# Optimization experiments

Hardware: AMD Instinct MI355X
Metric: run time of the kernel (lower is better)

The kernel has to match this reference:

```python
import jax, jax.numpy as jnp
import numpy as np

N_NODES = 100000
N_GRAPHS = 512


def gcn_conv(x, W, b, src, dst, n):
    # PyG GCNConv: h = x @ W; add self-loops; sym-normalize; scatter-add to dst; + bias
    h = x @ W
    loop = jnp.arange(n, dtype=src.dtype)
    s = jnp.concatenate([src, loop])
    d = jnp.concatenate([dst, loop])
    deg = jax.ops.segment_sum(jnp.ones_like(d, dtype=h.dtype), d, num_segments=n)
    dinv = jnp.where(deg > 0, jax.lax.rsqrt(deg), 0.0)
    norm = dinv[s] * dinv[d]               # [E+N]
    msg = h[s] * norm[:, None]             # gather + scale
    out = jax.ops.segment_sum(msg, d, num_segments=n)
    return out + b


def setup_inputs() -> dict:
    key = jax.random.key(0)
    ks = jax.random.split(key, 12)
    F_in, H, C = 128, 128, 10
    x = jax.random.normal(ks[0], (N_NODES, F_in), dtype=jnp.float32)
    edge_index = jax.random.randint(ks[1], (2, 3200000), 0, N_NODES, dtype=jnp.int64)
    batch = jnp.sort(jax.random.randint(ks[2], (N_NODES,), 0, N_GRAPHS, dtype=jnp.int64))
    def glorot(k, fi, fo):
        s = jnp.sqrt(6.0 / (fi + fo))
        return jax.random.uniform(k, (fi, fo), dtype=jnp.float32, minval=-s, maxval=s)
    return {
        "x": x, "edge_index": edge_index, "batch": batch,
        "W_in": glorot(ks[3], F_in, H), "b_in": jnp.zeros((H,), jnp.float32),
        "W_h0": glorot(ks[4], H, H), "b_h0": jnp.zeros((H,), jnp.float32),
        "W_h1": glorot(ks[5], H, H), "b_h1": jnp.zeros((H,), jnp.float32),
        "W_out": glorot(ks[6], H, C), "b_out": jnp.zeros((C,), jnp.float32),
    }


def reference(x, edge_index, batch, W_in, b_in, W_h0, b_h0, W_h1, b_h1, W_out, b_out):
    src, dst = edge_index[0], edge_index[1]
    n = x.shape[0]
    h = jax.nn.relu(gcn_conv(x, W_in, b_in, src, dst, n))
    h = jax.nn.relu(gcn_conv(h, W_h0, b_h0, src, dst, n))
    h = jax.nn.relu(gcn_conv(h, W_h1, b_h1, src, dst, n))
    h = gcn_conv(h, W_out, b_out, src, dst, n)
    # global_mean_pool over graph ids
    sums = jax.ops.segment_sum(h, batch, num_segments=N_GRAPHS)
    cnts = jax.ops.segment_sum(jnp.ones((n,), h.dtype), batch, num_segments=N_GRAPHS)
    pooled = sums / jnp.maximum(cnts, 1.0)[:, None]
    return jax.nn.log_softmax(pooled, axis=-1)
```

## Files before the change

### kernel.cpp

```cpp
#include <hip/hip_runtime.h>
#include <math.h>

#define TPB 256
#define MAXDEG 80
#define SHIFT 8
#define BNODES 256
#define EPB 4096
#define QB 32
#define LSTR 136

typedef short bf16x8 __attribute__((ext_vector_type(8)));
typedef float f32x4 __attribute__((ext_vector_type(4)));

__device__ inline unsigned short f2bf(float f) {
    unsigned u = __float_as_uint(f);
    return (unsigned short)((u + 0x7fffu + ((u >> 16) & 1u)) >> 16);
}
__device__ inline float bflo(unsigned u) { return __uint_as_float(u << 16); }
__device__ inline float bfhi(unsigned u) { return __uint_as_float(u & 0xffff0000u); }


__global__ __launch_bounds__(TPB) void p1_k(const int* __restrict__ src,
                                            const int* __restrict__ dst,
                                            int* __restrict__ cntmat,
                                            int* __restrict__ buckets,
                                            int E, int nb, int nblk1) {
    __shared__ int lcur[512];
    int tid = threadIdx.x, blk = blockIdx.x;
    for (int b = tid; b < nb; b += TPB) lcur[b] = 0;
    __syncthreads();
    int e0 = blk * EPB;
    int m = E - e0; if (m > EPB) m = EPB;
    for (int i = tid; i < m; i += TPB) {
        int d = dst[e0 + i];
        int s = src[e0 + i];
        int b = d >> SHIFT;
        int pos = atomicAdd(&lcur[b], 1);
        if (pos < QB)
            buckets[((size_t)b * nblk1 + blk) * QB + pos] = (s << SHIFT) | (d & (BNODES - 1));
    }
    __syncthreads();
    for (int b = tid; b < nb; b += TPB) {
        int c = lcur[b];
        cntmat[blk * nb + b] = c < QB ? c : QB;
    }
}


__global__ __launch_bounds__(TPB) void p2_k(const int* __restrict__ cntmat,
                                            const int* __restrict__ buckets,
                                            int* __restrict__ csr,
                                            int* __restrict__ deg,
                                            float* __restrict__ dinv, int n, int nb, int nblk1,
                                            const float* __restrict__ W0,
                                            const float* __restrict__ W1,
                                            const float* __restrict__ W2,
                                            const float* __restrict__ W3,
                                            unsigned short* __restrict__ T0,
                                            unsigned short* __restrict__ T1,
                                            unsigned short* __restrict__ T2,
                                            unsigned short* __restrict__ T3,
                                            float* __restrict__ pool,
                                            int* __restrict__ cnt, int ng) {
    int b = blockIdx.x, tid = threadIdx.x;
    if (b >= nb) {
        int widx = b - nb;
        if (widx < 3) {
            const float* W = widx == 0 ? W0 : (widx == 1 ? W1 : W2);
            unsigned short* T = widx == 0 ? T0 : (widx == 1 ? T1 : T2);
            for (int idx = tid; idx < 16384; idx += TPB) {
                int nn = idx >> 7, kk = idx & 127;
                T[idx] = f2bf(W[kk * 128 + nn]);
            }
        } else {
            for (int idx = tid; idx < 2048; idx += TPB) {
                int nn = idx >> 7, kk = idx & 127;
                T3[idx] = nn < 10 ? f2bf(W3[kk * 10 + nn]) : (unsigned short)0;
            }
            for (int i = tid; i < ng * 10; i += TPB) pool[i] = 0.f;
            for (int i = tid; i < ng; i += TPB) cnt[i] = 0;
        }
        return;
    }
    __shared__ int lcnt[BNODES];
    __shared__ int cnts[784];
    lcnt[tid] = 0;
    for (int blk = tid; blk < nblk1; blk += TPB) cnts[blk] = cntmat[blk * nb + b];
    __syncthreads();
    const int* bp = buckets + (size_t)b * nblk1 * QB;
    int vb = b << SHIFT;
    int tot = nblk1 * QB;
    for (int j = tid; j < tot; j += TPB) {
        int blk = j / QB;
        int i = j - blk * QB;
        if (i < cnts[blk]) {
            int rec = bp[(size_t)blk * QB + i];
            int dl = rec & (BNODES - 1);
            int pos = atomicAdd(&lcnt[dl], 1);
            if (pos < MAXDEG) csr[(size_t)(vb + dl) * MAXDEG + pos] = rec >> SHIFT;
        }
    }
    __syncthreads();
    int v = vb + tid;
    if (v < n) {
        int c = lcnt[tid];
        deg[v] = c < MAXDEG ? c : MAXDEG;
        dinv[v] = rsqrtf((float)(c + 1));
    }
}


__device__ __forceinline__ void mfma_tile(const unsigned short* Hs,
                                          const unsigned short* __restrict__ WT,
                                          const float* __restrict__ dinv,
                                          unsigned short* __restrict__ gout,
                                          int vb, int n, int w, int l) {
    f32x4 acc[2][8];
#pragma unroll
    for (int a = 0; a < 2; a++)
#pragma unroll
        for (int b = 0; b < 8; b++)
#pragma unroll
            for (int j = 0; j < 4; j++) acc[a][b][j] = 0.f;
    const int quad = l >> 4, lm = l & 15;
    const int mrow0 = w * 32;
#pragma unroll
    for (int ks = 0; ks < 4; ks++) {
        bf16x8 a0 = *(const bf16x8*)(Hs + (mrow0 + lm) * LSTR + ks * 32 + quad * 8);
        bf16x8 a1 = *(const bf16x8*)(Hs + (mrow0 + 16 + lm) * LSTR + ks * 32 + quad * 8);
#pragma unroll
        for (int nt = 0; nt < 8; nt++) {
            bf16x8 bf = *(const bf16x8*)(WT + (size_t)(nt * 16 + lm) * 128 + ks * 32 + quad * 8);
            acc[0][nt] = __builtin_amdgcn_mfma_f32_16x16x32_bf16(a0, bf, acc[0][nt], 0, 0, 0);
            acc[1][nt] = __builtin_amdgcn_mfma_f32_16x16x32_bf16(a1, bf, acc[1][nt], 0, 0, 0);
        }
    }
#pragma unroll
    for (int mt = 0; mt < 2; mt++) {
#pragma unroll
        for (int j = 0; j < 4; j++) {
            int r = vb + mrow0 + mt * 16 + quad * 4 + j;
            if (r < n) {
                float s = dinv[r];
#pragma unroll
                for (int nt = 0; nt < 8; nt++)
                    gout[(size_t)r * 128 + nt * 16 + lm] = f2bf(acc[mt][nt][j] * s);
            }
        }
    }
}


__global__ __launch_bounds__(256) void gemm_f32in(const float* __restrict__ x,
                                                  const unsigned short* __restrict__ WT,
                                                  const float* __restrict__ dinv,
                                                  unsigned short* __restrict__ gout, int n) {
    __shared__ unsigned short Hs[128 * LSTR];
    int tid = threadIdx.x;
    int vb = blockIdx.x * 128;
    for (int i = tid; i < 8192; i += 256) {
        int row = i >> 6, cw = i & 63;
        int gr = vb + row; if (gr > n - 1) gr = n - 1;
        float2 xv = *(const float2*)(x + (size_t)gr * 128 + cw * 2);
        unsigned pk = ((unsigned)f2bf(xv.y) << 16) | f2bf(xv.x);
        *(unsigned*)(Hs + row * LSTR + cw * 2) = pk;
    }
    __syncthreads();
    mfma_tile(Hs, WT, dinv, gout, vb, n, tid >> 6, tid & 63);
}


__global__ __launch_bounds__(256) void gemm_bf16in(const unsigned* __restrict__ hin,
                                                   const unsigned short* __restrict__ WT,
                                                   const float* __restrict__ dinv,
                                                   unsigned short* __restrict__ gout, int n) {
    __shared__ unsigned short Hs[128 * LSTR];
    int tid = threadIdx.x;
    int vb = blockIdx.x * 128;
    for (int i = tid; i < 8192; i += 256) {
        int row = i >> 6, cw = i & 63;
        int gr = vb + row; if (gr > n - 1) gr = n - 1;
        *(unsigned*)(Hs + row * LSTR + cw * 2) = hin[(size_t)gr * 64 + cw];
    }
    __syncthreads();
    mfma_tile(Hs, WT, dinv, gout, vb, n, tid >> 6, tid & 63);
}


__global__ __launch_bounds__(256) void thin_mfma(const unsigned* __restrict__ hin,
                                                 const unsigned short* __restrict__ WT3,
                                                 const float* __restrict__ dinv,
                                                 unsigned* __restrict__ g4u, int n) {
    __shared__ unsigned short Hs[128 * LSTR];
    int tid = threadIdx.x;
    int vb = blockIdx.x * 128;
    for (int i = tid; i < 8192; i += 256) {
        int row = i >> 6, cw = i & 63;
        int gr = vb + row; if (gr > n - 1) gr = n - 1;
        *(unsigned*)(Hs + row * LSTR + cw * 2) = hin[(size_t)gr * 64 + cw];
    }
    __syncthreads();
    int w = tid >> 6, l = tid & 63;
    int quad = l >> 4, lm = l & 15;
    int mrow0 = w * 32;
    f32x4 acc[2];
#pragma unroll
    for (int a = 0; a < 2; a++)
#pragma unroll
        for (int j = 0; j < 4; j++) acc[a][j] = 0.f;
#pragma unroll
    for (int ks = 0; ks < 4; ks++) {
        bf16x8 a0 = *(const bf16x8*)(Hs + (mrow0 + lm) * LSTR + ks * 32 + quad * 8);
        bf16x8 a1 = *(const bf16x8*)(Hs + (mrow0 + 16 + lm) * LSTR + ks * 32 + quad * 8);
        bf16x8 bf = *(const bf16x8*)(WT3 + (size_t)lm * 128 + ks * 32 + quad * 8);
        acc[0] = __builtin_amdgcn_mfma_f32_16x16x32_bf16(a0, bf, acc[0], 0, 0, 0);
        acc[1] = __builtin_amdgcn_mfma_f32_16x16x32_bf16(a1, bf, acc[1], 0, 0, 0);
    }
#pragma unroll
    for (int mt = 0; mt < 2; mt++) {
#pragma unroll
        for (int j = 0; j < 4; j++) {
            float self = acc[mt][j];
            float part = __shfl_down(self, 1, 64);
            int r = vb + mrow0 + mt * 16 + quad * 4 + j;
            if ((lm & 1) == 0 && lm < 10 && r < n) {
                float s = dinv[r];
                g4u[(size_t)r * 5 + (lm >> 1)] =
                    ((unsigned)f2bf(part * s) << 16) | f2bf(self * s);
            }
        }
    }
}


__global__ __launch_bounds__(256) void aggb_k(const unsigned* __restrict__ g,
                                              const float* __restrict__ dinv,
                                              const int* __restrict__ deg,
                                              const int* __restrict__ csr,
                                              const float* __restrict__ bias,
                                              unsigned* __restrict__ hout, int n) {
    int w = __builtin_amdgcn_readfirstlane((int)(threadIdx.x >> 6));
    int l = threadIdx.x & 63;
    int v = blockIdx.x * 4 + w;
    if (v >= n) return;
    unsigned u = g[(size_t)v * 64 + l];
    float acc0 = bflo(u), acc1 = bfhi(u);
    const int* cp = csr + (size_t)v * MAXDEG;
    int d = deg[v];
    int e = 0;
    for (; e + 8 <= d; e += 8) {
        int s0 = cp[e], s1 = cp[e + 1], s2 = cp[e + 2], s3 = cp[e + 3];
        int s4 = cp[e + 4], s5 = cp[e + 5], s6 = cp[e + 6], s7 = cp[e + 7];
        unsigned u0 = g[(size_t)s0 * 64 + l];
        unsigned u1 = g[(size_t)s1 * 64 + l];
        unsigned u2 = g[(size_t)s2 * 64 + l];
        unsigned u3 = g[(size_t)s3 * 64 + l];
        unsigned u4 = g[(size_t)s4 * 64 + l];
        unsigned u5 = g[(size_t)s5 * 64 + l];
        unsigned u6 = g[(size_t)s6 * 64 + l];
        unsigned u7 = g[(size_t)s7 * 64 + l];
        acc0 += (bflo(u0) + bflo(u1)) + (bflo(u2) + bflo(u3))
              + (bflo(u4) + bflo(u5)) + (bflo(u6) + bflo(u7));
        acc1 += (bfhi(u0) + bfhi(u1)) + (bfhi(u2) + bfhi(u3))
              + (bfhi(u4) + bfhi(u5)) + (bfhi(u6) + bfhi(u7));
    }
    for (; e < d; e++) {
        unsigned ux = g[(size_t)cp[e] * 64 + l];
        acc0 += bflo(ux); acc1 += bfhi(ux);
    }
    float2 bb = *(const float2*)(bias + 2 * l);
    float s = dinv[v];
    float o0 = fmaxf(s * acc0 + bb.x, 0.f);
    float o1 = fmaxf(s * acc1 + bb.y, 0.f);
    hout[(size_t)v * 64 + l] = ((unsigned)f2bf(o1) << 16) | f2bf(o0);
}


#define POOL_SPAN 8

__global__ __launch_bounds__(TPB) void agg_thin_pool(const unsigned* __restrict__ g4u,
                                                     const float* __restrict__ dinv,
                                                     const int* __restrict__ deg,
                                                     const int* __restrict__ csr,
                                                     const float* __restrict__ bias,
                                                     const int* __restrict__ batch,
                                                     float* __restrict__ pool,
                                                     int* __restrict__ cnt, int n) {
    __shared__ float lp[POOL_SPAN][10];
    __shared__ int lc[POOL_SPAN];
    __shared__ int g0s;
    int tid = threadIdx.x;
    int q = tid / 5, t = tid - q * 5;
    int v = blockIdx.x * 50 + q;
    if (tid == 0) {
        int f = blockIdx.x * 50;
        if (f > n - 1) f = n - 1;
        g0s = batch[f];
    }
    if (tid < POOL_SPAN) lc[tid] = 0;
    if (tid < POOL_SPAN * 10) lp[tid / 10][tid % 10] = 0.f;
    __syncthreads();
    if (tid < 250 && v < n) {
        unsigned u = g4u[(size_t)v * 5 + t];
        float acc0 = bflo(u), acc1 = bfhi(u);
        const int* cp = csr + (size_t)v * MAXDEG;
        int d = deg[v];
        int e = 0;
        for (; e + 4 <= d; e += 4) {
            unsigned u0 = g4u[(size_t)cp[e] * 5 + t];
            unsigned u1 = g4u[(size_t)cp[e + 1] * 5 + t];
            unsigned u2 = g4u[(size_t)cp[e + 2] * 5 + t];
            unsigned u3 = g4u[(size_t)cp[e + 3] * 5 + t];
            acc0 += (bflo(u0) + bflo(u1)) + (bflo(u2) + bflo(u3));
            acc1 += (bfhi(u0) + bfhi(u1)) + (bfhi(u2) + bfhi(u3));
        }
        for (; e < d; e++) {
            unsigned ux = g4u[(size_t)cp[e] * 5 + t];
            acc0 += bflo(ux); acc1 += bfhi(ux);
        }
        float s = dinv[v];
        float o0 = s * acc0 + bias[2 * t];
        float o1 = s * acc1 + bias[2 * t + 1];
        int gi = batch[v];
        int o = gi - g0s;
        if (o < POOL_SPAN) {
            if (t == 0) atomicAdd(&lc[o], 1);
            atomicAdd(&lp[o][2 * t], o0);
            atomicAdd(&lp[o][2 * t + 1], o1);
        } else {
            if (t == 0) atomicAdd(&cnt[gi], 1);
            atomicAdd(&pool[gi * 10 + 2 * t], o0);
            atomicAdd(&pool[gi * 10 + 2 * t + 1], o1);
        }
    }
    __syncthreads();
    if (tid < POOL_SPAN) {
        if (lc[tid] > 0) atomicAdd(&cnt[g0s + tid], lc[tid]);
    }
    if (tid < POOL_SPAN * 10) {
        int o = tid / 10, c = tid % 10;
        if (lc[o] > 0) atomicAdd(&pool[(g0s + o) * 10 + c], lp[o][c]);
    }
}

__global__ __launch_bounds__(TPB) void final_k(const float* __restrict__ pool,
                                               const int* __restrict__ cnt,
                                               float* __restrict__ out, int ng) {
    int gi = blockIdx.x * TPB + threadIdx.x;
    if (gi >= ng) return;
    float cn = fmaxf((float)cnt[gi], 1.f);
    float x[10];
    float m = -1e30f;
#pragma unroll
    for (int c = 0; c < 10; c++) {
        x[c] = pool[gi * 10 + c] / cn;
        m = fmaxf(m, x[c]);
    }
    float s = 0.f;
#pragma unroll
    for (int c = 0; c < 10; c++) s += expf(x[c] - m);
    float l = logf(s);
#pragma unroll
    for (int c = 0; c < 10; c++) out[gi * 10 + c] = x[c] - m - l;
}


extern "C" void kernel_launch(void* const* d_in, const int* in_sizes, int n_in,
                              void* d_out, int out_size, void* d_ws, size_t ws_size,
                              hipStream_t stream) {
    const float* x    = (const float*)d_in[0];
    const int*   ei   = (const int*)d_in[1];
    const int*   batch= (const int*)d_in[2];
    const float* W_in = (const float*)d_in[3];
    const float* b_in = (const float*)d_in[4];
    const float* W_h0 = (const float*)d_in[5];
    const float* b_h0 = (const float*)d_in[6];
    const float* W_h1 = (const float*)d_in[7];
    const float* b_h1 = (const float*)d_in[8];
    const float* W_out= (const float*)d_in[9];
    const float* b_out= (const float*)d_in[10];

    const int n  = in_sizes[2];
    const int E  = in_sizes[1] / 2;
    const int ng = out_size / 10;
    const int nb = (n + BNODES - 1) >> SHIFT;
    const int nblk1 = (E + EPB - 1) / EPB;

    char* p = (char*)d_ws;
    auto carve = [&](size_t bytes) { void* r = (void*)p; p += (bytes + 255) & ~(size_t)255; return r; };
    int*            deg    = (int*)           carve((size_t)n * 4);
    float*          dinv   = (float*)         carve((size_t)n * 4);
    int*            cntmat = (int*)           carve((size_t)nblk1 * nb * 4);
    int*            buckets= (int*)           carve((size_t)nb * nblk1 * QB * 4);
    int*            csr    = (int*)           carve((size_t)n * MAXDEG * 4);
    unsigned*       G      = (unsigned*)      carve((size_t)n * 64 * 4);
    unsigned*       H      = (unsigned*)      carve((size_t)n * 64 * 4);
    unsigned short* WT0    = (unsigned short*)carve(16384 * 2);
    unsigned short* WT1    = (unsigned short*)carve(16384 * 2);
    unsigned short* WT2    = (unsigned short*)carve(16384 * 2);
    unsigned short* WT3    = (unsigned short*)carve(2048 * 2);
    unsigned*       g4u    = (unsigned*)      carve((size_t)n * 5 * 4);
    float*          pool   = (float*)         carve((size_t)ng * 10 * 4);
    int*            cnt    = (int*)           carve((size_t)ng * 4);

    const int gG = (n + 127) / 128;
    const int gA4 = (n + 3) / 4;

    p1_k<<<nblk1, TPB, 0, stream>>>(ei, ei + E, cntmat, buckets, E, nb, nblk1);
    p2_k<<<nb + 4, TPB, 0, stream>>>(cntmat, buckets, csr, deg, dinv, n, nb, nblk1,
                                     W_in, W_h0, W_h1, W_out, WT0, WT1, WT2, WT3,
                                     pool, cnt, ng);

    gemm_f32in<<<gG, 256, 0, stream>>>(x, WT0, dinv, (unsigned short*)G, n);
    aggb_k<<<gA4, 256, 0, stream>>>(G, dinv, deg, csr, b_in, H, n);
    gemm_bf16in<<<gG, 256, 0, stream>>>(H, WT1, dinv, (unsigned short*)G, n);
    aggb_k<<<gA4, 256, 0, stream>>>(G, dinv, deg, csr, b_h0, H, n);
    gemm_bf16in<<<gG, 256, 0, stream>>>(H, WT2, dinv, (unsigned short*)G, n);
    aggb_k<<<gA4, 256, 0, stream>>>(G, dinv, deg, csr, b_h1, H, n);
    thin_mfma<<<gG, 256, 0, stream>>>(H, WT3, dinv, g4u, n);
    agg_thin_pool<<<(n + 49) / 50, TPB, 0, stream>>>(g4u, dinv, deg, csr, b_out, batch, pool, cnt, n);
    final_k<<<(ng + TPB - 1) / TPB, TPB, 0, stream>>>(pool, cnt, (float*)d_out, ng);
}
```

Baseline: 687.3 us.

## Replace per-block fixed-slot buckets with global atomic-reserved contiguous buckets

The edge partitioning pass now builds a per-block histogram of destination buckets and reserves contiguous ranges in a global per-bucket counter with one atomic per bucket. Edges are written densely into fixed-capacity bucket arrays. The CSR build then scans only the valid records instead of a sparse nblk1×QB grid with per-slot count checks. This removes wasted reads of empty slots and the count matrix, at the cost of an extra histogram pass over dst, global atomics, and a memset. Records beyond CAP per bucket are dropped, and the order of neighbours inside each bucket is no longer deterministic.

```diff
diff --git a/kernel.cpp b/kernel.cpp
--- a/kernel.cpp
+++ b/kernel.cpp
@@ -5,8 +5,8 @@
 #define MAXDEG 80
 #define SHIFT 8
 #define BNODES 256
+#define CAP 10240
 #define EPB 4096
-#define QB 32
 #define LSTR 136
 
 typedef short bf16x8 __attribute__((ext_vector_type(8)));
@@ -22,36 +22,38 @@
 
 __global__ __launch_bounds__(TPB) void p1_k(const int* __restrict__ src,
                                             const int* __restrict__ dst,
-                                            int* __restrict__ cntmat,
-                                            int* __restrict__ buckets,
-                                            int E, int nb, int nblk1) {
+                                            int* __restrict__ gbcnt,
+                                            int* __restrict__ buckets, int E, int nb) {
+    __shared__ int hist[512];
     __shared__ int lcur[512];
-    int tid = threadIdx.x, blk = blockIdx.x;
-    for (int b = tid; b < nb; b += TPB) lcur[b] = 0;
-    __syncthreads();
-    int e0 = blk * EPB;
+    int tid = threadIdx.x;
+    for (int b = tid; b < nb; b += TPB) hist[b] = 0;
+    __syncthreads();
+    int e0 = blockIdx.x * EPB;
     int m = E - e0; if (m > EPB) m = EPB;
+    for (int i = tid; i < m; i += TPB)
+        atomicAdd(&hist[dst[e0 + i] >> SHIFT], 1);
+    __syncthreads();
+    for (int b = tid; b < nb; b += TPB) {
+        int h = hist[b];
+        lcur[b] = h ? atomicAdd(&gbcnt[b], h) : 0;
+    }
+    __syncthreads();
     for (int i = tid; i < m; i += TPB) {
         int d = dst[e0 + i];
         int s = src[e0 + i];
         int b = d >> SHIFT;
         int pos = atomicAdd(&lcur[b], 1);
-        if (pos < QB)
-            buckets[((size_t)b * nblk1 + blk) * QB + pos] = (s << SHIFT) | (d & (BNODES - 1));
-    }
-    __syncthreads();
-    for (int b = tid; b < nb; b += TPB) {
-        int c = lcur[b];
-        cntmat[blk * nb + b] = c < QB ? c : QB;
-    }
-}
-
-
-__global__ __launch_bounds__(TPB) void p2_k(const int* __restrict__ cntmat,
+        if (pos < CAP) buckets[(size_t)b * CAP + pos] = (s << SHIFT) | (d & (BNODES - 1));
+    }
+}
+
+
+__global__ __launch_bounds__(TPB) void p2_k(const int* __restrict__ gbcnt,
                                             const int* __restrict__ buckets,
                                             int* __restrict__ csr,
                                             int* __restrict__ deg,
-                                            float* __restrict__ dinv, int n, int nb, int nblk1,
+                                            float* __restrict__ dinv, int n, int nb,
                                             const float* __restrict__ W0,
                                             const float* __restrict__ W1,
                                             const float* __restrict__ W2,
@@ -83,22 +85,16 @@
         return;
     }
     __shared__ int lcnt[BNODES];
-    __shared__ int cnts[784];
     lcnt[tid] = 0;
-    for (int blk = tid; blk < nblk1; blk += TPB) cnts[blk] = cntmat[blk * nb + b];
-    __syncthreads();
-    const int* bp = buckets + (size_t)b * nblk1 * QB;
+    __syncthreads();
+    int m = gbcnt[b]; if (m > CAP) m = CAP;
+    const int* bp = buckets + (size_t)b * CAP;
     int vb = b << SHIFT;
-    int tot = nblk1 * QB;
-    for (int j = tid; j < tot; j += TPB) {
-        int blk = j / QB;
-        int i = j - blk * QB;
-        if (i < cnts[blk]) {
-            int rec = bp[(size_t)blk * QB + i];
-            int dl = rec & (BNODES - 1);
-            int pos = atomicAdd(&lcnt[dl], 1);
-            if (pos < MAXDEG) csr[(size_t)(vb + dl) * MAXDEG + pos] = rec >> SHIFT;
-        }
+    for (int i = tid; i < m; i += TPB) {
+        int rec = bp[i];
+        int dl = rec & (BNODES - 1);
+        int pos = atomicAdd(&lcnt[dl], 1);
+        if (pos < MAXDEG) csr[(size_t)(vb + dl) * MAXDEG + pos] = rec >> SHIFT;
     }
     __syncthreads();
     int v = vb + tid;
@@ -384,14 +380,13 @@
     const int E  = in_sizes[1] / 2;
     const int ng = out_size / 10;
     const int nb = (n + BNODES - 1) >> SHIFT;
-    const int nblk1 = (E + EPB - 1) / EPB;
 
     char* p = (char*)d_ws;
     auto carve = [&](size_t bytes) { void* r = (void*)p; p += (bytes + 255) & ~(size_t)255; return r; };
     int*            deg    = (int*)           carve((size_t)n * 4);
     float*          dinv   = (float*)         carve((size_t)n * 4);
-    int*            cntmat = (int*)           carve((size_t)nblk1 * nb * 4);
-    int*            buckets= (int*)           carve((size_t)nb * nblk1 * QB * 4);
+    int*            gbcnt  = (int*)           carve((size_t)nb * 4);
+    int*            buckets= (int*)           carve((size_t)nb * CAP * 4);
     int*            csr    = (int*)           carve((size_t)n * MAXDEG * 4);
     unsigned*       G      = (unsigned*)      carve((size_t)n * 64 * 4);
     unsigned*       H      = (unsigned*)      carve((size_t)n * 64 * 4);
@@ -403,11 +398,14 @@
     float*          pool   = (float*)         carve((size_t)ng * 10 * 4);
     int*            cnt    = (int*)           carve((size_t)ng * 4);
 
+    (void)hipMemsetAsync(gbcnt, 0, (size_t)nb * 4, stream);
+
+    const int gP1 = (E + EPB - 1) / EPB;
     const int gG = (n + 127) / 128;
     const int gA4 = (n + 3) / 4;
 
-    p1_k<<<nblk1, TPB, 0, stream>>>(ei, ei + E, cntmat, buckets, E, nb, nblk1);
-    p2_k<<<nb + 4, TPB, 0, stream>>>(cntmat, buckets, csr, deg, dinv, n, nb, nblk1,
+    p1_k<<<gP1, TPB, 0, stream>>>(ei, ei + E, gbcnt, buckets, E, nb);
+    p2_k<<<nb + 4, TPB, 0, stream>>>(gbcnt, buckets, csr, deg, dinv, n, nb,
                                      W_in, W_h0, W_h1, W_out, WT0, WT1, WT2, WT3,
                                      pool, cnt, ng);
 
```

Result: faster. 648.2 us (-5.7%).
